# Optimization experiments

Hardware: AMD Instinct MI355X
Metric: run time of the kernel (lower is better)

The kernel has to match this reference:

```python
import jax, jax.numpy as jnp
import numpy as np
import math

D_MODEL = 512
NHEAD = 8
D_HEAD = D_MODEL // NHEAD
D_FF = 2048
N_LAYERS = 6
B, S = 8, 2048
EPS = 1e-5


def _layernorm(x, g, b):
    mu = jnp.mean(x, axis=-1, keepdims=True)
    var = jnp.mean(jnp.square(x - mu), axis=-1, keepdims=True)
    return (x - mu) * jax.lax.rsqrt(var + EPS) * g + b


def setup_inputs() -> dict:
    key = jax.random.key(0)
    ks = jax.random.split(key, 10)
    sc = 1.0 / math.sqrt(D_MODEL)
    scf = 1.0 / math.sqrt(D_FF)
    return {
        "x": jax.random.normal(ks[0], (B, S, D_MODEL), jnp.float32),
        "wq": jax.random.normal(ks[1], (N_LAYERS, D_MODEL, D_MODEL), jnp.float32) * sc,
        "wk": jax.random.normal(ks[2], (N_LAYERS, D_MODEL, D_MODEL), jnp.float32) * sc,
        "wv": jax.random.normal(ks[3], (N_LAYERS, D_MODEL, D_MODEL), jnp.float32) * sc,
        "wo": jax.random.normal(ks[4], (N_LAYERS, D_MODEL, D_MODEL), jnp.float32) * sc,
        "w1": jax.random.normal(ks[5], (N_LAYERS, D_MODEL, D_FF), jnp.float32) * sc,
        "b1": jnp.zeros((N_LAYERS, D_FF), jnp.float32),
        "w2": jax.random.normal(ks[6], (N_LAYERS, D_FF, D_MODEL), jnp.float32) * scf,
        "b2": jnp.zeros((N_LAYERS, D_MODEL), jnp.float32),
        "g1": jnp.ones((N_LAYERS, D_MODEL), jnp.float32),
        "beta1": jnp.zeros((N_LAYERS, D_MODEL), jnp.float32),
        "g2": jnp.ones((N_LAYERS, D_MODEL), jnp.float32),
        "beta2": jnp.zeros((N_LAYERS, D_MODEL), jnp.float32),
    }


def reference(x, wq, wk, wv, wo, w1, b1, w2, b2, g1, beta1, g2, beta2):
    scale = 1.0 / math.sqrt(D_HEAD)
    for i in range(N_LAYERS):
        # NOTE: faithful to torch .view(B, nhead, -1, d_head) WITHOUT transpose
        q = (x @ wq[i]).reshape(B, NHEAD, S, D_HEAD)
        k = (x @ wk[i]).reshape(B, NHEAD, S, D_HEAD)
        v = (x @ wv[i]).reshape(B, NHEAD, S, D_HEAD)
        u = jnp.einsum("bhsd,bhtd->bhst", q, k) * scale
        attn = jax.nn.softmax(u, axis=-1)
        o = jnp.einsum("bhst,bhtd->bhsd", attn, v).reshape(B, S, D_MODEL)
        x = _layernorm(x + o @ wo[i], g1[i], beta1[i])
        f = jax.nn.relu(x @ w1[i] + b1[i]) @ w2[i] + b2[i]
        x = _layernorm(x + f, g2[i], beta2[i])
    return x
```

## Files before the change

### kernel.cpp

```cpp
#include <hip/hip_runtime.h>
#include <hip/hip_bf16.h>
#include <stdint.h>

typedef __bf16 bf16_t;
typedef bf16_t bf16x8 __attribute__((ext_vector_type(8)));
typedef bf16_t bf16x4 __attribute__((ext_vector_type(4)));
typedef float  f32x4  __attribute__((ext_vector_type(4)));

#define AS1 __attribute__((address_space(1)))
#define AS3 __attribute__((address_space(3)))

__device__ __forceinline__ void gload_lds16(const void* g, void* l) {
  __builtin_amdgcn_global_load_lds((const AS1 void*)g, (AS3 void*)l, 16, 0, 0);
}

__device__ __forceinline__ float fast_exp2(float x) {
#if __has_builtin(__builtin_amdgcn_exp2f)
  return __builtin_amdgcn_exp2f(x);
#else
  return exp2f(x);
#endif
}

#define QSCALE 0.1803368801111204f

template <int RELU, int BIAS, int QKV, int DBUF>
__global__ __launch_bounds__(256) void gemm_bt(const bf16_t* __restrict__ A,
                                               const bf16_t* __restrict__ Bt,
                                               const float* __restrict__ bias,
                                               bf16_t* __restrict__ Cv,
                                               int M, int N, int K, int ldc) {
  __shared__ __align__(16) char smem[DBUF ? 65536 : 32768];
  const int t = threadIdx.x;
  const int l = t & 63;
  const int w = t >> 6;
  const int wm = w >> 1, wn = w & 1;
  const int lr = l & 15, lg = l >> 4;

  const int gx = gridDim.x;
  const int nwg = gx * gridDim.y;
  const int orig = blockIdx.y * gx + blockIdx.x;
  const int swz = (orig & 7) * (nwg >> 3) + (orig >> 3);
  const long m0 = (long)(swz / gx) * 128;
  const long n0 = (long)(swz % gx) * 128;

  const bf16_t* asrc[4];
  const bf16_t* bsrc[4];
#pragma unroll
  for (int it = 0; it < 4; ++it) {
    int y = it * 4096 + t * 16;
    int row = y >> 7;
    int col = ((y & 127) ^ ((row & 7) << 4)) >> 1;
    asrc[it] = A + (m0 + row) * (long)K + col;
    bsrc[it] = Bt + (n0 + row) * (long)K + col;
  }

  auto stage = [&](int buf) {
    char* sb = smem + buf * 32768;
#pragma unroll
    for (int it = 0; it < 4; ++it) {
      gload_lds16(asrc[it], sb + it * 4096 + t * 16);
      gload_lds16(bsrc[it], sb + 16384 + it * 4096 + t * 16);
      asrc[it] += 64;
      bsrc[it] += 64;
    }
  };

  f32x4 acc[4][4] = {};
  const int nt = K >> 6;

  auto compute = [&](char* sb) {
#pragma unroll
    for (int kk = 0; kk < 2; ++kk) {
      const int c2 = (kk * 32 + lg * 8) * 2;
      bf16x8 a[4], b[4];
#pragma unroll
      for (int i = 0; i < 4; ++i) {
        int ra = wm * 64 + i * 16 + lr;
        a[i] = *(const bf16x8*)(sb + ((ra * 128 + c2) ^ ((ra & 7) << 4)));
        int rb = wn * 64 + i * 16 + lr;
        b[i] = *(const bf16x8*)(sb + 16384 + ((rb * 128 + c2) ^ ((rb & 7) << 4)));
      }
      __builtin_amdgcn_s_setprio(1);
#pragma unroll
      for (int i = 0; i < 4; ++i)
#pragma unroll
        for (int j = 0; j < 4; ++j)
          acc[i][j] = __builtin_amdgcn_mfma_f32_16x16x32_bf16(a[i], b[j], acc[i][j], 0, 0, 0);
      __builtin_amdgcn_s_setprio(0);
    }
  };

  if (DBUF) {
    stage(0);
    __syncthreads();
    int buf = 0;
    for (int kt = 0; kt < nt; ++kt) {
      if (kt + 1 < nt) stage(buf ^ 1);
      compute(smem + buf * 32768);
      __syncthreads();
      buf ^= 1;
    }
  } else {
    for (int kt = 0; kt < nt; ++kt) {
      __syncthreads();
      stage(0);
      __syncthreads();
      compute(smem);
    }
  }

  float bv[4];
  if (BIAS) {
#pragma unroll
    for (int j = 0; j < 4; ++j) bv[j] = bias[n0 + wn * 64 + j * 16 + lr];
  }
#pragma unroll
  for (int i = 0; i < 4; ++i) {
    long rowb = m0 + wm * 64 + i * 16 + lg * 4;
#pragma unroll
    for (int j = 0; j < 4; ++j) {
      int colbase = (int)n0 + wn * 64 + j * 16;
      bf16_t* outp;
      int coll;
      if (QKV) {
        outp = Cv + (size_t)(colbase >> 9) * 8388608;
        coll = (colbase & 511) + lr;
      } else {
        outp = Cv;
        coll = colbase + lr;
      }
#pragma unroll
      for (int r = 0; r < 4; ++r) {
        float v = acc[i][j][r];
        if (BIAS) v += bv[j];
        if (RELU) v = v > 0.f ? v : 0.f;
        outp[(rowb + r) * (long)ldc + coll] = (bf16_t)v;
      }
    }
  }
}

template <int BIAS, int FINAL>
__global__ __launch_bounds__(512) void gemm_resln(const bf16_t* __restrict__ A,
                                                  const bf16_t* __restrict__ Bt,
                                                  const float* __restrict__ bias,
                                                  bf16_t* __restrict__ xb,
                                                  float* __restrict__ xout,
                                                  const float* __restrict__ g,
                                                  const float* __restrict__ be,
                                                  int K) {
  __shared__ __align__(16) char smem[147456];
  const int t = threadIdx.x, l = t & 63, w = t >> 6;
  const int lr = l & 15, lg = l >> 4;
  const int orig = blockIdx.x;
  const int swz = (orig & 7) * 32 + (orig >> 3);
  const long m0 = (long)swz * 64;

  const bf16_t* src[9];
#pragma unroll
  for (int i = 0; i < 9; ++i) {
    int gy = i * 8192 + t * 16;
    if (gy < 8192) {
      int row = gy >> 7;
      int col = ((gy & 127) ^ ((row & 7) << 4)) >> 1;
      src[i] = A + (m0 + row) * (long)K + col;
    } else {
      int by = gy - 8192;
      int row = by >> 7;
      int col = ((by & 127) ^ ((row & 7) << 4)) >> 1;
      src[i] = Bt + (long)row * K + col;
    }
  }
  auto stage = [&](int buf) {
    char* sb = smem + buf * 73728;
#pragma unroll
    for (int i = 0; i < 9; ++i) {
      gload_lds16(src[i], sb + i * 8192 + t * 16);
      src[i] += 64;
    }
  };

  f32x4 acc[4][4] = {};
  const int nt = K >> 6;
  stage(0);
  __syncthreads();
  int buf = 0;
  for (int kt = 0; kt < nt; ++kt) {
    if (kt + 1 < nt) stage(buf ^ 1);
    char* sb = smem + buf * 73728;
#pragma unroll
    for (int kk = 0; kk < 2; ++kk) {
      const int c2 = (kk * 32 + lg * 8) * 2;
      bf16x8 a[4], b[4];
#pragma unroll
      for (int i = 0; i < 4; ++i) {
        int ra = i * 16 + lr;
        a[i] = *(const bf16x8*)(sb + ((ra * 128 + c2) ^ ((ra & 7) << 4)));
        int rb = w * 64 + i * 16 + lr;
        b[i] = *(const bf16x8*)(sb + 8192 + ((rb * 128 + c2) ^ ((rb & 7) << 4)));
      }
      __builtin_amdgcn_s_setprio(1);
#pragma unroll
      for (int i = 0; i < 4; ++i)
#pragma unroll
        for (int j = 0; j < 4; ++j)
          acc[i][j] = __builtin_amdgcn_mfma_f32_16x16x32_bf16(a[i], b[j], acc[i][j], 0, 0, 0);
      __builtin_amdgcn_s_setprio(0);
    }
    __syncthreads();
    buf ^= 1;
  }

  float* lnsum = (float*)smem;
  float* lnsq  = (float*)(smem + 2048);
  float* lnm   = (float*)(smem + 4096);
  float* lnr   = (float*)(smem + 4352);

  float bv[4];
  if (BIAS) {
#pragma unroll
    for (int j = 0; j < 4; ++j) bv[j] = bias[w * 64 + j * 16 + lr];
  }
  float sv[4][4][4];
#pragma unroll
  for (int i = 0; i < 4; ++i)
#pragma unroll
    for (int r = 0; r < 4; ++r) {
      long row = m0 + i * 16 + lg * 4 + r;
#pragma unroll
      for (int j = 0; j < 4; ++j) {
        float d = acc[i][j][r];
        if (BIAS) d += bv[j];
        float xold = (float)xb[row * 512 + w * 64 + j * 16 + lr];
        sv[i][r][j] = xold + d;
      }
    }
#pragma unroll
  for (int i = 0; i < 4; ++i)
#pragma unroll
    for (int r = 0; r < 4; ++r) {
      float ps = sv[i][r][0] + sv[i][r][1] + sv[i][r][2] + sv[i][r][3];
      float pq = sv[i][r][0] * sv[i][r][0] + sv[i][r][1] * sv[i][r][1] +
                 sv[i][r][2] * sv[i][r][2] + sv[i][r][3] * sv[i][r][3];
#pragma unroll
      for (int m = 1; m <= 8; m <<= 1) {
        ps += __shfl_xor(ps, m, 64);
        pq += __shfl_xor(pq, m, 64);
      }
      if (lr == 0) {
        int rl = i * 16 + lg * 4 + r;
        lnsum[rl * 8 + w] = ps;
        lnsq[rl * 8 + w] = pq;
      }
    }
  __syncthreads();
  if (t < 64) {
    float s8 = 0.f, q8 = 0.f;
#pragma unroll
    for (int wv = 0; wv < 8; ++wv) {
      s8 += lnsum[t * 8 + wv];
      q8 += lnsq[t * 8 + wv];
    }
    float mu = s8 * (1.f / 512.f);
    float var = q8 * (1.f / 512.f) - mu * mu;
    lnm[t] = mu;
    lnr[t] = rsqrtf(var + 1e-5f);
  }
  __syncthreads();
  float gv[4], bev[4];
#pragma unroll
  for (int j = 0; j < 4; ++j) {
    gv[j] = g[w * 64 + j * 16 + lr];
    bev[j] = be[w * 64 + j * 16 + lr];
  }
#pragma unroll
  for (int i = 0; i < 4; ++i)
#pragma unroll
    for (int r = 0; r < 4; ++r) {
      int rl = i * 16 + lg * 4 + r;
      long row = m0 + rl;
      float mu = lnm[rl], rstd = lnr[rl];
#pragma unroll
      for (int j = 0; j < 4; ++j) {
        int col = w * 64 + j * 16 + lr;
        float y = (sv[i][r][j] - mu) * rstd * gv[j] + bev[j];
        xb[row * 512 + col] = (bf16_t)y;
        if (FINAL) xout[row * 512 + col] = y;
      }
    }
}

__global__ __launch_bounds__(512) void attn_fa(const bf16_t* __restrict__ qg,
                                               const bf16_t* __restrict__ kg,
                                               const bf16_t* __restrict__ vg,
                                               bf16_t* __restrict__ og) {
  __shared__ __align__(16) char smem[81920];
  const int t = threadIdx.x, l = t & 63, w = t >> 6;
  const int lr = l & 15, lg = l >> 4;
  const int lin = blockIdx.x;
  const int swz = (lin & 7) * 64 + (lin >> 3);
  const long hoff = (long)(swz >> 3) * 131072;
  const int q0 = (swz & 7) * 256 + w * 32;
  const uint32_t LDSB = (uint32_t)(uintptr_t)(AS3 char*)smem;

  bf16x8 qf[2][2];
#pragma unroll
  for (int nf = 0; nf < 2; ++nf)
#pragma unroll
    for (int kk = 0; kk < 2; ++kk)
      qf[nf][kk] = *(const bf16x8*)(qg + hoff + (long)(q0 + nf * 16 + lr) * 64 + kk * 32 + lg * 8);

  const bf16_t* ksrc;
  {
    int y = t * 16;
    int row = y >> 7;
    int col = ((y & 127) ^ ((row & 7) << 4)) >> 1;
    ksrc = kg + hoff + (long)row * 64 + col;
  }
  const bf16_t* vsrc;
  {
    int y = t * 16;
    int kk = y >> 12;
    int nj = (y >> 10) & 3;
    int jhi = (y >> 9) & 1;
    int lgs = (y >> 7) & 3;
    int r = (y >> 5) & 3;
    int ch = (y >> 4) & 1;
    int kv = kk * 32 + jhi * 16 + lgs * 4 + r;
    int d0 = nj * 16 + ch * 8;
    vsrc = vg + hoff + (long)kv * 64 + d0;
  }

  auto stage = [&](int buf) {
    char* sb = smem + buf * 16384;
    gload_lds16(ksrc, sb + t * 16);
    gload_lds16(vsrc, sb + 8192 + t * 16);
    ksrc += 4096;
    vsrc += 4096;
  };

  f32x4 oacc[2][4] = {};
  f32x4 lacc[2] = {};
  bf16x8 onesf;
#pragma unroll
  for (int j = 0; j < 8; ++j) onesf[j] = (bf16_t)1.0f;

  auto tile_compute = [&](int bufIdx) {
    char* sb = smem + bufIdx * 16384;
    f32x4 sT[4][2] = {};
#pragma unroll
    for (int kk = 0; kk < 2; ++kk) {
      const int c2 = (kk * 32 + lg * 8) * 2;
      bf16x8 kf[4];
#pragma unroll
      for (int mf = 0; mf < 4; ++mf) {
        int rk = mf * 16 + lr;
        kf[mf] = *(const bf16x8*)(sb + ((rk * 128 + c2) ^ ((rk & 7) << 4)));
      }
      __builtin_amdgcn_s_setprio(1);
#pragma unroll
      for (int mf = 0; mf < 4; ++mf)
#pragma unroll
        for (int nf = 0; nf < 2; ++nf)
          sT[mf][nf] = __builtin_amdgcn_mfma_f32_16x16x32_bf16(kf[mf], qf[nf][kk], sT[mf][nf], 0, 0, 0);
      __builtin_amdgcn_s_setprio(0);
    }

    uint32_t va = LDSB + (uint32_t)bufIdx * 16384u + 8192u + (uint32_t)l * 8u;
    bf16x4 tv0, tv1, tv2, tv3, tv4, tv5, tv6, tv7;
    bf16x4 tv8, tv9, tva, tvb, tvc, tvd, tve, tvf;
    asm volatile(
        "ds_read_b64_tr_b16 %0, %16 offset:0\n\t"
        "ds_read_b64_tr_b16 %1, %16 offset:512\n\t"
        "ds_read_b64_tr_b16 %2, %16 offset:1024\n\t"
        "ds_read_b64_tr_b16 %3, %16 offset:1536\n\t"
        "ds_read_b64_tr_b16 %4, %16 offset:2048\n\t"
        "ds_read_b64_tr_b16 %5, %16 offset:2560\n\t"
        "ds_read_b64_tr_b16 %6, %16 offset:3072\n\t"
        "ds_read_b64_tr_b16 %7, %16 offset:3584\n\t"
        "ds_read_b64_tr_b16 %8, %16 offset:4096\n\t"
        "ds_read_b64_tr_b16 %9, %16 offset:4608\n\t"
        "ds_read_b64_tr_b16 %10, %16 offset:5120\n\t"
        "ds_read_b64_tr_b16 %11, %16 offset:5632\n\t"
        "ds_read_b64_tr_b16 %12, %16 offset:6144\n\t"
        "ds_read_b64_tr_b16 %13, %16 offset:6656\n\t"
        "ds_read_b64_tr_b16 %14, %16 offset:7168\n\t"
        "ds_read_b64_tr_b16 %15, %16 offset:7680"
        : "=&v"(tv0), "=&v"(tv1), "=&v"(tv2), "=&v"(tv3),
          "=&v"(tv4), "=&v"(tv5), "=&v"(tv6), "=&v"(tv7),
          "=&v"(tv8), "=&v"(tv9), "=&v"(tva), "=&v"(tvb),
          "=&v"(tvc), "=&v"(tvd), "=&v"(tve), "=&v"(tvf)
        : "v"(va));

    bf16x8 pa[2][2];
#pragma unroll
    for (int m2 = 0; m2 < 2; ++m2)
#pragma unroll
      for (int kk = 0; kk < 2; ++kk) {
        f32x4 e0, e1;
#pragma unroll
        for (int r = 0; r < 4; ++r) {
          e0[r] = fast_exp2(sT[2 * kk][m2][r]);
          e1[r] = fast_exp2(sT[2 * kk + 1][m2][r]);
        }
        bf16x4 c0 = __builtin_convertvector(e0, bf16x4);
        bf16x4 c1 = __builtin_convertvector(e1, bf16x4);
        pa[m2][kk] = __builtin_shufflevector(c0, c1, 0, 1, 2, 3, 4, 5, 6, 7);
      }

    asm volatile("s_waitcnt lgkmcnt(0)" ::: "memory");
    __builtin_amdgcn_sched_barrier(0);

    bf16x8 vf[2][4];
    vf[0][0] = __builtin_shufflevector(tv0, tv1, 0, 1, 2, 3, 4, 5, 6, 7);
    vf[0][1] = __builtin_shufflevector(tv2, tv3, 0, 1, 2, 3, 4, 5, 6, 7);
    vf[0][2] = __builtin_shufflevector(tv4, tv5, 0, 1, 2, 3, 4, 5, 6, 7);
    vf[0][3] = __builtin_shufflevector(tv6, tv7, 0, 1, 2, 3, 4, 5, 6, 7);
    vf[1][0] = __builtin_shufflevector(tv8, tv9, 0, 1, 2, 3, 4, 5, 6, 7);
    vf[1][1] = __builtin_shufflevector(tva, tvb, 0, 1, 2, 3, 4, 5, 6, 7);
    vf[1][2] = __builtin_shufflevector(tvc, tvd, 0, 1, 2, 3, 4, 5, 6, 7);
    vf[1][3] = __builtin_shufflevector(tve, tvf, 0, 1, 2, 3, 4, 5, 6, 7);

    __builtin_amdgcn_s_setprio(1);
#pragma unroll
    for (int kk = 0; kk < 2; ++kk)
#pragma unroll
      for (int m2 = 0; m2 < 2; ++m2) {
#pragma unroll
        for (int nj = 0; nj < 4; ++nj)
          oacc[m2][nj] = __builtin_amdgcn_mfma_f32_16x16x32_bf16(pa[m2][kk], vf[kk][nj], oacc[m2][nj], 0, 0, 0);
        lacc[m2] = __builtin_amdgcn_mfma_f32_16x16x32_bf16(pa[m2][kk], onesf, lacc[m2], 0, 0, 0);
      }
    __builtin_amdgcn_s_setprio(0);
  };

  stage(0);
  stage(1);
  stage(2);
  int nxt = 3;
  for (int i = 0; i < 16; ++i) {
    if (i == 15) asm volatile("s_waitcnt vmcnt(0)" ::: "memory");
    else         asm volatile("s_waitcnt vmcnt(2)" ::: "memory");
    asm volatile("s_barrier" ::: "memory");
    if (nxt < 32) { stage(nxt % 5); ++nxt; }
    if (nxt < 32) { stage(nxt % 5); ++nxt; }
    tile_compute((2 * i) % 5);
    tile_compute((2 * i + 1) % 5);
  }

#pragma unroll
  for (int m2 = 0; m2 < 2; ++m2)
#pragma unroll
    for (int r = 0; r < 4; ++r) {
      float inv = 1.f / lacc[m2][r];
      long row = q0 + m2 * 16 + lg * 4 + r;
#pragma unroll
      for (int nj = 0; nj < 4; ++nj)
        og[hoff + row * 64 + nj * 16 + lr] = (bf16_t)(oacc[m2][nj][r] * inv);
    }
}

__global__ __launch_bounds__(256) void transpose_w(const float* __restrict__ src,
                                                   bf16_t* __restrict__ dst,
                                                   int K, int N,
                                                   long dstLayerStride, float scale) {
  __shared__ float tile[32][33];
  const int t = threadIdx.x;
  const int tx = t & 31, ty = t >> 5;
  const long ls = (long)blockIdx.z * K * N;
  const long ld = (long)blockIdx.z * dstLayerStride;
  const int n0 = blockIdx.x * 32, k0 = blockIdx.y * 32;
#pragma unroll
  for (int i = 0; i < 4; ++i)
    tile[ty + i * 8][tx] = src[ls + (long)(k0 + ty + i * 8) * N + n0 + tx];
  __syncthreads();
#pragma unroll
  for (int i = 0; i < 4; ++i)
    dst[ld + (long)(n0 + ty + i * 8) * K + k0 + tx] = (bf16_t)(tile[tx][ty + i * 8] * scale);
}

__global__ __launch_bounds__(256) void init_x(const float* __restrict__ x,
                                              bf16_t* __restrict__ xb) {
  long i = ((long)blockIdx.x * 256 + threadIdx.x) * 8;
  f32x4 a = *(const f32x4*)(x + i);
  f32x4 b = *(const f32x4*)(x + i + 4);
  bf16x8 o;
#pragma unroll
  for (int j = 0; j < 4; ++j) { o[j] = (bf16_t)a[j]; o[4 + j] = (bf16_t)b[j]; }
  *(bf16x8*)(xb + i) = o;
}

extern "C" void kernel_launch(void* const* d_in, const int* in_sizes, int n_in,
                              void* d_out, int out_size, void* d_ws, size_t ws_size,
                              hipStream_t stream) {
  const float* x = (const float*)d_in[0];
  const float* wq = (const float*)d_in[1];
  const float* wk = (const float*)d_in[2];
  const float* wv = (const float*)d_in[3];
  const float* wo = (const float*)d_in[4];
  const float* w1 = (const float*)d_in[5];
  const float* b1 = (const float*)d_in[6];
  const float* w2 = (const float*)d_in[7];
  const float* b2 = (const float*)d_in[8];
  const float* g1 = (const float*)d_in[9];
  const float* be1 = (const float*)d_in[10];
  const float* g2 = (const float*)d_in[11];
  const float* be2 = (const float*)d_in[12];

  char* ws = (char*)d_ws;

  const int M = 16384, D = 512, DFF = 2048, NL = 6;
  const size_t sz_small = (size_t)NL * D * D * 2;
  const size_t sz_big = (size_t)NL * D * DFF * 2;
  bf16_t* wqkvt = (bf16_t*)(ws);
  bf16_t* wot = (bf16_t*)(ws + 3 * sz_small);
  bf16_t* w1t = (bf16_t*)(ws + 4 * sz_small);
  bf16_t* w2t = (bf16_t*)(ws + 4 * sz_small + sz_big);
  char* actbase = ws + 4 * sz_small + 2 * sz_big;
  bf16_t* xb = (bf16_t*)(actbase);
  char* R = actbase + (size_t)M * D * 2;
  bf16_t* qb = (bf16_t*)(R);
  bf16_t* kb = (bf16_t*)(R + (size_t)M * D * 2);
  bf16_t* vb = (bf16_t*)(R + 2 * (size_t)M * D * 2);
  bf16_t* ob = (bf16_t*)(R + 3 * (size_t)M * D * 2);
  bf16_t* hb = (bf16_t*)(R);

  const long LQKV = 1536L * 512;
  transpose_w<<<dim3(D / 32, D / 32, NL), 256, 0, stream>>>(wq, wqkvt, D, D, LQKV, QSCALE);
  transpose_w<<<dim3(D / 32, D / 32, NL), 256, 0, stream>>>(wk, wqkvt + 512 * 512, D, D, LQKV, 1.f);
  transpose_w<<<dim3(D / 32, D / 32, NL), 256, 0, stream>>>(wv, wqkvt + 2 * 512 * 512, D, D, LQKV, 1.f);
  transpose_w<<<dim3(D / 32, D / 32, NL), 256, 0, stream>>>(wo, wot, D, D, (long)D * D, 1.f);
  transpose_w<<<dim3(DFF / 32, D / 32, NL), 256, 0, stream>>>(w1, w1t, D, DFF, (long)D * DFF, 1.f);
  transpose_w<<<dim3(D / 32, DFF / 32, NL), 256, 0, stream>>>(w2, w2t, DFF, D, (long)D * DFF, 1.f);
  init_x<<<4096, 256, 0, stream>>>(x, xb);

  for (int L = 0; L < NL; ++L) {
    const bf16_t* wqkvL = wqkvt + (size_t)L * LQKV;
    const bf16_t* woL = wot + (size_t)L * D * D;
    const bf16_t* w1L = w1t + (size_t)L * D * DFF;
    const bf16_t* w2L = w2t + (size_t)L * D * DFF;

    gemm_bt<0, 0, 1, 0><<<dim3(12, 128), 256, 0, stream>>>(xb, wqkvL, nullptr, qb, M, 1536, D, 512);
    attn_fa<<<dim3(512), 512, 0, stream>>>(qb, kb, vb, ob);
    gemm_resln<0, 0><<<dim3(256), 512, 0, stream>>>(ob, woL, nullptr, xb, nullptr,
                                                    g1 + L * D, be1 + L * D, D);
    gemm_bt<1, 1, 0, 0><<<dim3(16, 128), 256, 0, stream>>>(xb, w1L, b1 + (size_t)L * DFF, hb, M, DFF, D, DFF);
    if (L == NL - 1)
      gemm_resln<1, 1><<<dim3(256), 512, 0, stream>>>(hb, w2L, b2 + L * D, xb, (float*)d_out,
                                                      g2 + L * D, be2 + L * D, DFF);
    else
      gemm_resln<1, 0><<<dim3(256), 512, 0, stream>>>(hb, w2L, b2 + L * D, xb, nullptr,
                                                      g2 + L * D, be2 + L * D, DFF);
  }
}
```

Before: 1.403 ms.

## Refine attention KV pipeline waits and merge four weight transposes into one launch

The attention loop now waits only for the tile it is about to compute, with a split vmcnt wait between the two tile computes, instead of draining down to two outstanding loads per iteration. The tail is peeled explicitly so the last tiles use tighter waits. The aim is to let more KV loads stay in flight while MFMA work runs. Separately, the four square weight transposes become one kernel launch, removing three launches from the setup. The finer vmcnt counts depend on the exact number of loads each stage issues and could cause races if they are miscounted.

```diff
diff --git a/kernel.cpp b/kernel.cpp
--- a/kernel.cpp
+++ b/kernel.cpp
@@ -9,6 +9,9 @@
 
 #define AS1 __attribute__((address_space(1)))
 #define AS3 __attribute__((address_space(3)))
+
+#define WAITV(n) asm volatile("s_waitcnt vmcnt(" #n ")" ::: "memory")
+#define SBAR() asm volatile("s_barrier" ::: "memory")
 
 __device__ __forceinline__ void gload_lds16(const void* g, void* l) {
   __builtin_amdgcn_global_load_lds((const AS1 void*)g, (AS3 void*)l, 16, 0, 0);
@@ -439,15 +442,26 @@
   stage(1);
   stage(2);
   int nxt = 3;
-  for (int i = 0; i < 16; ++i) {
-    if (i == 15) asm volatile("s_waitcnt vmcnt(0)" ::: "memory");
-    else         asm volatile("s_waitcnt vmcnt(2)" ::: "memory");
-    asm volatile("s_barrier" ::: "memory");
-    if (nxt < 32) { stage(nxt % 5); ++nxt; }
-    if (nxt < 32) { stage(nxt % 5); ++nxt; }
+  for (int i = 0; i < 14; ++i) {
+    WAITV(4);
+    SBAR();
+    stage(nxt % 5); ++nxt;
+    stage(nxt % 5); ++nxt;
     tile_compute((2 * i) % 5);
+    WAITV(6);
     tile_compute((2 * i + 1) % 5);
   }
+  WAITV(4);
+  SBAR();
+  stage(31 % 5);
+  tile_compute(28 % 5);
+  WAITV(4);
+  tile_compute(29 % 5);
+  WAITV(2);
+  SBAR();
+  tile_compute(30 % 5);
+  WAITV(0);
+  tile_compute(31 % 5);
 
 #pragma unroll
   for (int m2 = 0; m2 < 2; ++m2)
@@ -478,6 +492,35 @@
 #pragma unroll
   for (int i = 0; i < 4; ++i)
     dst[ld + (long)(n0 + ty + i * 8) * K + k0 + tx] = (bf16_t)(tile[tx][ty + i * 8] * scale);
+}
+
+__global__ __launch_bounds__(256) void transpose_w4(const float* __restrict__ wq,
+                                                    const float* __restrict__ wk,
+                                                    const float* __restrict__ wv,
+                                                    const float* __restrict__ wo,
+                                                    bf16_t* __restrict__ wqkvt,
+                                                    bf16_t* __restrict__ wot) {
+  __shared__ float tile[32][33];
+  const int t = threadIdx.x;
+  const int tx = t & 31, ty = t >> 5;
+  const int z = blockIdx.z, L = z >> 2, which = z & 3;
+  const float* src;
+  bf16_t* dst;
+  float scale = 1.f;
+  const long LQKV = 1536L * 512;
+  if (which == 0) { src = wq; dst = wqkvt + (long)L * LQKV; scale = QSCALE; }
+  else if (which == 1) { src = wk; dst = wqkvt + (long)L * LQKV + 512 * 512; }
+  else if (which == 2) { src = wv; dst = wqkvt + (long)L * LQKV + 2 * 512 * 512; }
+  else { src = wo; dst = wot + (long)L * 512 * 512; }
+  src += (long)L * 512 * 512;
+  const int n0 = blockIdx.x * 32, k0 = blockIdx.y * 32;
+#pragma unroll
+  for (int i = 0; i < 4; ++i)
+    tile[ty + i * 8][tx] = src[(long)(k0 + ty + i * 8) * 512 + n0 + tx];
+  __syncthreads();
+#pragma unroll
+  for (int i = 0; i < 4; ++i)
+    dst[(long)(n0 + ty + i * 8) * 512 + k0 + tx] = (bf16_t)(tile[tx][ty + i * 8] * scale);
 }
 
 __global__ __launch_bounds__(256) void init_x(const float* __restrict__ x,
@@ -527,19 +570,16 @@
   bf16_t* hb = (bf16_t*)(R);
 
   const long LQKV = 1536L * 512;
-  transpose_w<<<dim3(D / 32, D / 32, NL), 256, 0, stream>>>(wq, wqkvt, D, D, LQKV, QSCALE);
-  transpose_w<<<dim3(D / 32, D / 32, NL), 256, 0, stream>>>(wk, wqkvt + 512 * 512, D, D, LQKV, 1.f);
-  transpose_w<<<dim3(D / 32, D / 32, NL), 256, 0, stream>>>(wv, wqkvt + 2 * 512 * 512, D, D, LQKV, 1.f);
-  transpose_w<<<dim3(D / 32, D / 32, NL), 256, 0, stream>>>(wo, wot, D, D, (long)D * D, 1.f);
+  transpose_w4<<<dim3(16, 16, 24), 256, 0, stream>>>(wq, wk, wv, wo, wqkvt, wot);
   transpose_w<<<dim3(DFF / 32, D / 32, NL), 256, 0, stream>>>(w1, w1t, D, DFF, (long)D * DFF, 1.f);
   transpose_w<<<dim3(D / 32, DFF / 32, NL), 256, 0, stream>>>(w2, w2t, DFF, D, (long)D * DFF, 1.f);
   init_x<<<4096, 256, 0, stream>>>(x, xb);
 
   for (int L = 0; L < NL; ++L) {
     const bf16_t* wqkvL = wqkvt + (size_t)L * LQKV;
-    const bf16_t* woL = wot + (size_t)L * D * D;
     const bf16_t* w1L = w1t + (size_t)L * D * DFF;
     const bf16_t* w2L = w2t + (size_t)L * D * DFF;
+    const bf16_t* woL = wot + (size_t)L * D * D;
 
     gemm_bt<0, 0, 1, 0><<<dim3(12, 128), 256, 0, stream>>>(xb, wqkvL, nullptr, qb, M, 1536, D, 512);
     attn_fa<<<dim3(512), 512, 0, stream>>>(qb, kb, vb, ob);
```

Result: no change. 1.394 ms (-0.6%).
